# Kernel tuning notes

Measured on AMD Instinct MI355X. Metric: run time of the kernel, lower is better.

Reference implementation:

```python
import jax, jax.numpy as jnp
import numpy as np

N_NODES = 100000
N_EDGES = 3200000


def _gcn_layer(x, W, b, src, dst, n_nodes):
    # GCNConv: x' = D^{-1/2} (A + I) D^{-1/2} X W + b  (self-loops included in src/dst)
    h = x @ W  # [N, F_out]
    ones = jnp.ones(src.shape[0], dtype=x.dtype)
    deg = jax.ops.segment_sum(ones, dst, num_segments=n_nodes)  # in-degree incl. self-loop
    dinv = jnp.where(deg > 0, jax.lax.rsqrt(deg), 0.0)
    norm = dinv[src] * dinv[dst]  # [E+N]
    msg = h[src] * norm[:, None]  # gather + scale
    out = jax.ops.segment_sum(msg, dst, num_segments=n_nodes)  # scatter-add
    return out + b


def setup_inputs() -> dict:
    key = jax.random.key(0)
    k1, k2, k3, k4 = jax.random.split(key, 4)
    x = jax.random.normal(k1, (N_NODES, 64), dtype=jnp.float32)
    edge_index = jax.random.randint(k2, (2, N_EDGES), 0, N_NODES, dtype=jnp.int64)
    W1 = jax.random.normal(k3, (64, 128), dtype=jnp.float32) * (1.0 / np.sqrt(64))
    b1 = jnp.zeros((128,), dtype=jnp.float32)
    W2 = jax.random.normal(k4, (128, 64), dtype=jnp.float32) * (1.0 / np.sqrt(128))
    b2 = jnp.zeros((64,), dtype=jnp.float32)
    return {"x": x, "edge_index": edge_index, "W1": W1, "b1": b1, "W2": W2, "b2": b2}


def reference(x, edge_index, W1, b1, W2, b2):
    n = x.shape[0]
    loop = jnp.arange(n, dtype=edge_index.dtype)
    src = jnp.concatenate([edge_index[0], loop])
    dst = jnp.concatenate([edge_index[1], loop])
    h = _gcn_layer(x, W1, b1, src, dst, n)
    h = jax.nn.relu(h)
    # dropout is identity in eval mode (training=False)
    out = _gcn_layer(h, W2, b2, src, dst, n)
    return out
```

## Files before the change

kernel.cpp:

```cpp
#include <hip/hip_runtime.h>
#include <hip/hip_fp16.h>

#define N_NODES 100000
#define N_EDGES 3200000

#define NBLK_P 320
#define SLICE4 (N_EDGES / 4 / NBLK_P)
#define NBKT 256
#define BSHIFT 9
#define NBKT_USED ((N_NODES + 511) / 512)
#define EL_CAP 24576

struct alignas(8) Half4 { __half2 lo, hi; };


__global__ __launch_bounds__(256) void k_coarse_hist(const int4* __restrict__ dst4,
                                                     int* __restrict__ blockHist) {
    __shared__ int h[NBKT];
    int t = threadIdx.x;
    h[t] = 0;
    __syncthreads();
    int base = blockIdx.x * SLICE4;
    for (int i = t; i < SLICE4; i += 256) {
        int4 d = dst4[base + i];
        atomicAdd(&h[d.x >> BSHIFT], 1);
        atomicAdd(&h[d.y >> BSHIFT], 1);
        atomicAdd(&h[d.z >> BSHIFT], 1);
        atomicAdd(&h[d.w >> BSHIFT], 1);
    }
    __syncthreads();
    blockHist[blockIdx.x * NBKT + t] = h[t];
}

__global__ __launch_bounds__(1024) void k_colscan(int* __restrict__ blockHist,
                                                  int* __restrict__ coarseStart) {
    __shared__ int part[4][NBKT];
    __shared__ int s[NBKT];
    __shared__ int totA[NBKT];
    int tid = threadIdx.x;
    int b = tid & 255, q = tid >> 8;
    const int QR = NBLK_P / 4;
    int sum = 0;
    for (int r = q * QR; r < (q + 1) * QR; ++r) sum += blockHist[r * NBKT + b];
    part[q][b] = sum;
    __syncthreads();
    if (q == 0) {
        int tot = part[0][b] + part[1][b] + part[2][b] + part[3][b];
        s[b] = tot;
        totA[b] = tot;
    }
    __syncthreads();
    for (int off = 1; off < NBKT; off <<= 1) {
        int v = 0;
        if (q == 0 && b >= off) v = s[b - off];
        __syncthreads();
        if (q == 0) s[b] += v;
        __syncthreads();
    }
    int excl = s[b] - totA[b];
    if (q == 0) {
        coarseStart[b] = excl;
        if (b == 0) coarseStart[NBKT] = N_EDGES;
    }
    int run = excl;
    if (q > 0) run += part[0][b];
    if (q > 1) run += part[1][b];
    if (q > 2) run += part[2][b];
    for (int r = q * QR; r < (q + 1) * QR; ++r) {
        int v = blockHist[r * NBKT + b];
        blockHist[r * NBKT + b] = run;
        run += v;
    }
}

__global__ __launch_bounds__(256) void k_partition(const int4* __restrict__ src4,
                                                   const int4* __restrict__ dst4,
                                                   const int* __restrict__ blockHist,
                                                   int* __restrict__ sorted) {
    __shared__ int cur[NBKT];
    int t = threadIdx.x;
    cur[t] = blockHist[blockIdx.x * NBKT + t];
    __syncthreads();
    int base = blockIdx.x * SLICE4;
    for (int i = t; i < SLICE4; i += 256) {
        int4 d = dst4[base + i];
        int4 s = src4[base + i];
        int p;
        p = atomicAdd(&cur[d.x >> BSHIFT], 1); sorted[p] = s.x | ((d.x & 511) << 17);
        p = atomicAdd(&cur[d.y >> BSHIFT], 1); sorted[p] = s.y | ((d.y & 511) << 17);
        p = atomicAdd(&cur[d.z >> BSHIFT], 1); sorted[p] = s.z | ((d.z & 511) << 17);
        p = atomicAdd(&cur[d.w >> BSHIFT], 1); sorted[p] = s.w | ((d.w & 511) << 17);
    }
}

__global__ __launch_bounds__(256) void k_fine(const int* __restrict__ sorted,
                                              const int* __restrict__ coarseStart,
                                              const float4* __restrict__ x4,
                                              int* __restrict__ rowstart,
                                              float* __restrict__ dinvg,
                                              int* __restrict__ csr_src,
                                              Half4* __restrict__ xs) {
    __shared__ int eL[EL_CAP];
    __shared__ int h[512];
    __shared__ int pairsc[256];
    __shared__ int offs[512];
    __shared__ float dloc[512];
    int t = threadIdx.x;
    int bkt = blockIdx.x;
    int beg = coarseStart[bkt], end = coarseStart[bkt + 1];
    int cnt = end - beg;
    bool inLds = (cnt <= EL_CAP);
    h[t] = 0; h[t + 256] = 0;
    __syncthreads();
    if (inLds) {
        for (int i = t; i < cnt; i += 256) eL[i] = sorted[beg + i];
        __syncthreads();
        for (int i = t; i < cnt; i += 256) atomicAdd(&h[eL[i] >> 17], 1);
    } else {
        for (int i = beg + t; i < end; i += 256) atomicAdd(&h[sorted[i] >> 17], 1);
    }
    __syncthreads();
    int pv = h[2 * t] + h[2 * t + 1];
    pairsc[t] = pv;
    __syncthreads();
    for (int off = 1; off < 256; off <<= 1) {
        int v = (t >= off) ? pairsc[t - off] : 0;
        __syncthreads();
        pairsc[t] += v;
        __syncthreads();
    }
    int e0 = pairsc[t] - pv;
    offs[2 * t] = e0;
    offs[2 * t + 1] = e0 + h[2 * t];
    __syncthreads();
    int n0 = bkt << BSHIFT;
    int nvalid = N_NODES - n0;
    if (nvalid > 512) nvalid = 512;
#pragma unroll
    for (int q = 0; q < 2; ++q) {
        int local = t + q * 256;
        if (local < nvalid) {
            rowstart[n0 + local] = beg + offs[local];
            float dv = rsqrtf((float)(h[local] + 1));
            dloc[local] = dv;
            dinvg[n0 + local] = dv;
        }
    }
    if (bkt == 0 && t == 0) rowstart[N_NODES] = N_EDGES;
    __syncthreads();
    if (inLds) {
        for (int i = t; i < cnt; i += 256) {
            int pk = eL[i];
            int p = atomicAdd(&offs[pk >> 17], 1);
            csr_src[beg + p] = pk & 0x1FFFF;
        }
    } else {
        for (int i = beg + t; i < end; i += 256) {
            int pk = sorted[i];
            int p = atomicAdd(&offs[pk >> 17], 1);
            csr_src[beg + p] = pk & 0x1FFFF;
        }
    }
    for (int i = t; i < nvalid * 16; i += 256) {
        int local = i >> 4;
        int qq = i & 15;
        float d = dloc[local];
        float4 v = x4[(long long)(n0 + local) * 16 + qq];
        Half4 hh;
        hh.lo = __float22half2_rn(make_float2(v.x * d, v.y * d));
        hh.hi = __float22half2_rn(make_float2(v.z * d, v.w * d));
        xs[(long long)(n0 + local) * 16 + qq] = hh;
    }
}


__global__ __launch_bounds__(256) void k_gather_h(
    const int* __restrict__ rowstart, const int* __restrict__ csr_src,
    const float* __restrict__ dinv, const int4* __restrict__ xs16,
    const float4* __restrict__ bias4, float4* __restrict__ out4)
{
    int node = blockIdx.x * 4 + (threadIdx.x >> 6);
    if (node >= N_NODES) return;
    int lane = threadIdx.x & 63;
    int qlane = lane & 7;
    int egrp = lane >> 3;
    int beg = rowstart[node];
    int deg = rowstart[node + 1] - beg;
    float acc[8];
#pragma unroll
    for (int k = 0; k < 8; ++k) acc[k] = 0.f;
    if (egrp == 0) {
        int4 v = xs16[((long long)node << 3) + qlane];
        float2 f0 = __half22float2(*(__half2*)&v.x);
        float2 f1 = __half22float2(*(__half2*)&v.y);
        float2 f2 = __half22float2(*(__half2*)&v.z);
        float2 f3 = __half22float2(*(__half2*)&v.w);
        acc[0] = f0.x; acc[1] = f0.y; acc[2] = f1.x; acc[3] = f1.y;
        acc[4] = f2.x; acc[5] = f2.y; acc[6] = f3.x; acc[7] = f3.y;
    }
    for (int base = 0; base < deg; base += 64) {
        int rem = deg - base;
        if (rem > 64) rem = 64;
        int mye = (lane < rem) ? csr_src[beg + base + lane] : 0;
        int nj = (rem + 7) >> 3;
        for (int j = 0; j < nj; ++j) {
            int eidx = (j << 3) + egrp;
            int s = __shfl(mye, eidx);
            if (eidx < rem) {
                int4 v = xs16[((long long)s << 3) + qlane];
                float2 f0 = __half22float2(*(__half2*)&v.x);
                float2 f1 = __half22float2(*(__half2*)&v.y);
                float2 f2 = __half22float2(*(__half2*)&v.z);
                float2 f3 = __half22float2(*(__half2*)&v.w);
                acc[0] += f0.x; acc[1] += f0.y; acc[2] += f1.x; acc[3] += f1.y;
                acc[4] += f2.x; acc[5] += f2.y; acc[6] += f3.x; acc[7] += f3.y;
            }
        }
    }
#pragma unroll
    for (int k = 0; k < 8; ++k) {
        acc[k] += __shfl_xor(acc[k], 8);
        acc[k] += __shfl_xor(acc[k], 16);
        acc[k] += __shfl_xor(acc[k], 32);
    }
    if (egrp == 0) {
        float d = dinv[node];
        float4 b0 = bias4 ? bias4[qlane * 2] : make_float4(0.f, 0.f, 0.f, 0.f);
        float4 b1 = bias4 ? bias4[qlane * 2 + 1] : make_float4(0.f, 0.f, 0.f, 0.f);
        out4[(long long)node * 16 + qlane * 2] =
            make_float4(d * acc[0] + b0.x, d * acc[1] + b0.y, d * acc[2] + b0.z, d * acc[3] + b0.w);
        out4[(long long)node * 16 + qlane * 2 + 1] =
            make_float4(d * acc[4] + b1.x, d * acc[5] + b1.y, d * acc[6] + b1.z, d * acc[7] + b1.w);
    }
}


#define GTILE 128
__global__ __launch_bounds__(256) void k_fused_gemm(
    const float* __restrict__ A, const float* __restrict__ W1,
    const float* __restrict__ b1, const float* __restrict__ W2,
    const float* __restrict__ dinv, Half4* __restrict__ P)
{
    __shared__ float sBuf[128][GTILE];
    int tid = threadIdx.x;
    int R0 = blockIdx.x * GTILE;

    {
        int row = tid >> 1;
        int kb = (tid & 1) * 32;
        int grow = R0 + row;
        if (grow < N_NODES) {
            const float4* src = (const float4*)&A[(long long)grow * 64 + kb];
#pragma unroll
            for (int q = 0; q < 8; ++q) {
                float4 v = src[q];
                int k = kb + q * 4;
                sBuf[k + 0][row] = v.x;
                sBuf[k + 1][row] = v.y;
                sBuf[k + 2][row] = v.z;
                sBuf[k + 3][row] = v.w;
            }
        } else {
#pragma unroll
            for (int q = 0; q < 8; ++q) {
                int k = kb + q * 4;
                sBuf[k + 0][row] = 0.f; sBuf[k + 1][row] = 0.f;
                sBuf[k + 2][row] = 0.f; sBuf[k + 3][row] = 0.f;
            }
        }
    }
    __syncthreads();

    int rg = tid & 15;
    int cg = tid >> 4;
    int r0 = rg * 8;

    float acc[8][8];
#pragma unroll
    for (int i = 0; i < 8; ++i)
#pragma unroll
        for (int j = 0; j < 8; ++j) acc[i][j] = 0.f;
    {
        int c0 = cg * 8;
#pragma unroll 4
        for (int k = 0; k < 64; ++k) {
            float4 a0 = *(const float4*)&sBuf[k][r0];
            float4 a1 = *(const float4*)&sBuf[k][r0 + 4];
            float4 w0 = *(const float4*)&W1[k * 128 + c0];
            float4 w1 = *(const float4*)&W1[k * 128 + c0 + 4];
            float av[8] = {a0.x, a0.y, a0.z, a0.w, a1.x, a1.y, a1.z, a1.w};
            float wv[8] = {w0.x, w0.y, w0.z, w0.w, w1.x, w1.y, w1.z, w1.w};
#pragma unroll
            for (int i = 0; i < 8; ++i)
#pragma unroll
                for (int j = 0; j < 8; ++j) acc[i][j] += av[i] * wv[j];
        }
    }
    __syncthreads();

    {
        int c0 = cg * 8;
#pragma unroll
        for (int j = 0; j < 8; ++j) {
            float bb = b1[c0 + j];
            float4 h0, h1;
            h0.x = fmaxf(acc[0][j] + bb, 0.f);
            h0.y = fmaxf(acc[1][j] + bb, 0.f);
            h0.z = fmaxf(acc[2][j] + bb, 0.f);
            h0.w = fmaxf(acc[3][j] + bb, 0.f);
            h1.x = fmaxf(acc[4][j] + bb, 0.f);
            h1.y = fmaxf(acc[5][j] + bb, 0.f);
            h1.z = fmaxf(acc[6][j] + bb, 0.f);
            h1.w = fmaxf(acc[7][j] + bb, 0.f);
            *(float4*)&sBuf[c0 + j][r0] = h0;
            *(float4*)&sBuf[c0 + j][r0 + 4] = h1;
        }
    }
    __syncthreads();

    {
        int c0 = cg * 4;
        float acc2[8][4];
#pragma unroll
        for (int i = 0; i < 8; ++i)
#pragma unroll
            for (int j = 0; j < 4; ++j) acc2[i][j] = 0.f;
#pragma unroll 4
        for (int k = 0; k < 128; ++k) {
            float4 a0 = *(const float4*)&sBuf[k][r0];
            float4 a1 = *(const float4*)&sBuf[k][r0 + 4];
            float4 w = *(const float4*)&W2[k * 64 + c0];
            float av[8] = {a0.x, a0.y, a0.z, a0.w, a1.x, a1.y, a1.z, a1.w};
            float wv[4] = {w.x, w.y, w.z, w.w};
#pragma unroll
            for (int i = 0; i < 8; ++i)
#pragma unroll
                for (int j = 0; j < 4; ++j) acc2[i][j] += av[i] * wv[j];
        }
#pragma unroll
        for (int i = 0; i < 8; ++i) {
            int row = R0 + r0 + i;
            if (row < N_NODES) {
                float d = dinv[row];
                Half4 h;
                h.lo = __float22half2_rn(make_float2(d * acc2[i][0], d * acc2[i][1]));
                h.hi = __float22half2_rn(make_float2(d * acc2[i][2], d * acc2[i][3]));
                P[(long long)row * 16 + cg] = h;
            }
        }
    }
}


extern "C" void kernel_launch(void* const* d_in, const int* in_sizes, int n_in,
                              void* d_out, int out_size, void* d_ws, size_t ws_size,
                              hipStream_t stream) {
    const float* x  = (const float*)d_in[0];
    const int*   ei = (const int*)d_in[1];
    const float* W1 = (const float*)d_in[2];
    const float* b1 = (const float*)d_in[3];
    const float* W2 = (const float*)d_in[4];
    const float* b2 = (const float*)d_in[5];
    float* out = (float*)d_out;

    const int* srcE = ei;
    const int* dstE = ei + N_EDGES;

    char* w = (char*)d_ws;
    int*   blockHist   = (int*)w;   w += sizeof(int) * NBLK_P * NBKT;
    int*   coarseStart = (int*)w;   w += sizeof(int) * (NBKT + 1);
    int*   rowstart    = (int*)w;   w += sizeof(int) * (N_NODES + 8);
    float* dinv        = (float*)w; w += sizeof(float) * (N_NODES + 8);
    int*   csr_src     = (int*)w;   w += sizeof(int) * N_EDGES;
    Half4* xs          = (Half4*)w; w += sizeof(Half4) * (size_t)N_NODES * 16;
    int*   sorted      = (int*)w;
    float* agg1        = (float*)w; w += sizeof(float) * (size_t)N_NODES * 64;
    Half4* p2 = xs;

    k_coarse_hist<<<NBLK_P, 256, 0, stream>>>((const int4*)dstE, blockHist);
    k_colscan<<<1, 1024, 0, stream>>>(blockHist, coarseStart);
    k_partition<<<NBLK_P, 256, 0, stream>>>((const int4*)srcE, (const int4*)dstE,
                                            blockHist, sorted);
    k_fine<<<NBKT_USED, 256, 0, stream>>>(sorted, coarseStart, (const float4*)x,
                                          rowstart, dinv, csr_src, xs);

    k_gather_h<<<(N_NODES + 3) / 4, 256, 0, stream>>>(rowstart, csr_src, dinv,
                                                      (const int4*)xs, nullptr,
                                                      (float4*)agg1);
    k_fused_gemm<<<(N_NODES + GTILE - 1) / GTILE, 256, 0, stream>>>(agg1, W1, b1, W2, dinv, p2);

    k_gather_h<<<(N_NODES + 3) / 4, 256, 0, stream>>>(rowstart, csr_src, dinv,
                                                      (const int4*)p2, (const float4*)b2,
                                                      (float4*)out);
}
```

Measured before the change: 314.0 us.

## Split gathers into feature halves, store layer-1 aggregate in fp16, use finer buckets

```diff
diff --git a/kernel.cpp b/kernel.cpp
--- a/kernel.cpp
+++ b/kernel.cpp
@@ -6,19 +6,17 @@
 
 #define NBLK_P 320
 #define SLICE4 (N_EDGES / 4 / NBLK_P)
-#define NBKT 256
-#define BSHIFT 9
-#define NBKT_USED ((N_NODES + 511) / 512)
-#define EL_CAP 24576
-
-struct alignas(8) Half4 { __half2 lo, hi; };
+#define NBKT 512
+#define BSHIFT 8
+#define NBKT_USED ((N_NODES + 255) / 256)
+#define EL_CAP 12288
 
 
 __global__ __launch_bounds__(256) void k_coarse_hist(const int4* __restrict__ dst4,
                                                      int* __restrict__ blockHist) {
     __shared__ int h[NBKT];
     int t = threadIdx.x;
-    h[t] = 0;
+    h[t] = 0; h[t + 256] = 0;
     __syncthreads();
     int base = blockIdx.x * SLICE4;
     for (int i = t; i < SLICE4; i += 256) {
@@ -30,22 +28,23 @@
     }
     __syncthreads();
     blockHist[blockIdx.x * NBKT + t] = h[t];
+    blockHist[blockIdx.x * NBKT + t + 256] = h[t + 256];
 }
 
 __global__ __launch_bounds__(1024) void k_colscan(int* __restrict__ blockHist,
                                                   int* __restrict__ coarseStart) {
-    __shared__ int part[4][NBKT];
+    __shared__ int part[2][NBKT];
     __shared__ int s[NBKT];
     __shared__ int totA[NBKT];
     int tid = threadIdx.x;
-    int b = tid & 255, q = tid >> 8;
-    const int QR = NBLK_P / 4;
+    int b = tid & 511, q = tid >> 9;
+    const int QR = NBLK_P / 2;
     int sum = 0;
     for (int r = q * QR; r < (q + 1) * QR; ++r) sum += blockHist[r * NBKT + b];
     part[q][b] = sum;
     __syncthreads();
     if (q == 0) {
-        int tot = part[0][b] + part[1][b] + part[2][b] + part[3][b];
+        int tot = part[0][b] + part[1][b];
         s[b] = tot;
         totA[b] = tot;
     }
@@ -63,9 +62,7 @@
         if (b == 0) coarseStart[NBKT] = N_EDGES;
     }
     int run = excl;
-    if (q > 0) run += part[0][b];
-    if (q > 1) run += part[1][b];
-    if (q > 2) run += part[2][b];
+    if (q == 1) run += part[0][b];
     for (int r = q * QR; r < (q + 1) * QR; ++r) {
         int v = blockHist[r * NBKT + b];
         blockHist[r * NBKT + b] = run;
@@ -80,16 +77,17 @@
     __shared__ int cur[NBKT];
     int t = threadIdx.x;
     cur[t] = blockHist[blockIdx.x * NBKT + t];
+    cur[t + 256] = blockHist[blockIdx.x * NBKT + t + 256];
     __syncthreads();
     int base = blockIdx.x * SLICE4;
     for (int i = t; i < SLICE4; i += 256) {
         int4 d = dst4[base + i];
         int4 s = src4[base + i];
         int p;
-        p = atomicAdd(&cur[d.x >> BSHIFT], 1); sorted[p] = s.x | ((d.x & 511) << 17);
-        p = atomicAdd(&cur[d.y >> BSHIFT], 1); sorted[p] = s.y | ((d.y & 511) << 17);
-        p = atomicAdd(&cur[d.z >> BSHIFT], 1); sorted[p] = s.z | ((d.z & 511) << 17);
-        p = atomicAdd(&cur[d.w >> BSHIFT], 1); sorted[p] = s.w | ((d.w & 511) << 17);
+        p = atomicAdd(&cur[d.x >> BSHIFT], 1); sorted[p] = s.x | ((d.x & 255) << 17);
+        p = atomicAdd(&cur[d.y >> BSHIFT], 1); sorted[p] = s.y | ((d.y & 255) << 17);
+        p = atomicAdd(&cur[d.z >> BSHIFT], 1); sorted[p] = s.z | ((d.z & 255) << 17);
+        p = atomicAdd(&cur[d.w >> BSHIFT], 1); sorted[p] = s.w | ((d.w & 255) << 17);
     }
 }
 
@@ -99,18 +97,18 @@
                                               int* __restrict__ rowstart,
                                               float* __restrict__ dinvg,
                                               int* __restrict__ csr_src,
-                                              Half4* __restrict__ xs) {
+                                              int4* __restrict__ xs) {
     __shared__ int eL[EL_CAP];
-    __shared__ int h[512];
+    __shared__ int h[256];
     __shared__ int pairsc[256];
-    __shared__ int offs[512];
-    __shared__ float dloc[512];
+    __shared__ int offs[256];
+    __shared__ float dloc[256];
     int t = threadIdx.x;
     int bkt = blockIdx.x;
     int beg = coarseStart[bkt], end = coarseStart[bkt + 1];
     int cnt = end - beg;
     bool inLds = (cnt <= EL_CAP);
-    h[t] = 0; h[t + 256] = 0;
+    h[t] = 0;
     __syncthreads();
     if (inLds) {
         for (int i = t; i < cnt; i += 256) eL[i] = sorted[beg + i];
@@ -120,7 +118,7 @@
         for (int i = beg + t; i < end; i += 256) atomicAdd(&h[sorted[i] >> 17], 1);
     }
     __syncthreads();
-    int pv = h[2 * t] + h[2 * t + 1];
+    int pv = h[t];
     pairsc[t] = pv;
     __syncthreads();
     for (int off = 1; off < 256; off <<= 1) {
@@ -130,21 +128,15 @@
         __syncthreads();
     }
     int e0 = pairsc[t] - pv;
-    offs[2 * t] = e0;
-    offs[2 * t + 1] = e0 + h[2 * t];
-    __syncthreads();
+    offs[t] = e0;
     int n0 = bkt << BSHIFT;
     int nvalid = N_NODES - n0;
-    if (nvalid > 512) nvalid = 512;
-#pragma unroll
-    for (int q = 0; q < 2; ++q) {
-        int local = t + q * 256;
-        if (local < nvalid) {
-            rowstart[n0 + local] = beg + offs[local];
-            float dv = rsqrtf((float)(h[local] + 1));
-            dloc[local] = dv;
-            dinvg[n0 + local] = dv;
-        }
+    if (nvalid > 256) nvalid = 256;
+    if (t < nvalid) {
+        rowstart[n0 + t] = beg + e0;
+        float dv = rsqrtf((float)(pv + 1));
+        dloc[t] = dv;
+        dinvg[n0 + t] = dv;
     }
     if (bkt == 0 && t == 0) rowstart[N_NODES] = N_EDGES;
     __syncthreads();
@@ -166,31 +158,28 @@
         int qq = i & 15;
         float d = dloc[local];
         float4 v = x4[(long long)(n0 + local) * 16 + qq];
-        Half4 hh;
-        hh.lo = __float22half2_rn(make_float2(v.x * d, v.y * d));
-        hh.hi = __float22half2_rn(make_float2(v.z * d, v.w * d));
-        xs[(long long)(n0 + local) * 16 + qq] = hh;
-    }
-}
-
-
-__global__ __launch_bounds__(256) void k_gather_h(
+        __half2 lo = __float22half2_rn(make_float2(v.x * d, v.y * d));
+        __half2 hi = __float22half2_rn(make_float2(v.z * d, v.w * d));
+        int4 pk;
+        pk.x = *(int*)&lo;
+        pk.y = *(int*)&hi;
+        ((int2*)xs)[(long long)(n0 + local) * 16 + qq] = make_int2(pk.x, pk.y);
+    }
+}
+
+
+__device__ __forceinline__ void gather_half_core(
     const int* __restrict__ rowstart, const int* __restrict__ csr_src,
-    const float* __restrict__ dinv, const int4* __restrict__ xs16,
-    const float4* __restrict__ bias4, float4* __restrict__ out4)
+    const int4* __restrict__ xs8, int hoff, int node, int lane, float acc[8])
 {
-    int node = blockIdx.x * 4 + (threadIdx.x >> 6);
-    if (node >= N_NODES) return;
-    int lane = threadIdx.x & 63;
-    int qlane = lane & 7;
-    int egrp = lane >> 3;
+    int q = lane & 3;
+    int eg = lane >> 2;
     int beg = rowstart[node];
     int deg = rowstart[node + 1] - beg;
-    float acc[8];
 #pragma unroll
     for (int k = 0; k < 8; ++k) acc[k] = 0.f;
-    if (egrp == 0) {
-        int4 v = xs16[((long long)node << 3) + qlane];
+    if (eg == 0) {
+        int4 v = xs8[((long long)node << 3) + hoff + q];
         float2 f0 = __half22float2(*(__half2*)&v.x);
         float2 f1 = __half22float2(*(__half2*)&v.y);
         float2 f2 = __half22float2(*(__half2*)&v.z);
@@ -202,12 +191,12 @@
         int rem = deg - base;
         if (rem > 64) rem = 64;
         int mye = (lane < rem) ? csr_src[beg + base + lane] : 0;
-        int nj = (rem + 7) >> 3;
+        int nj = (rem + 15) >> 4;
         for (int j = 0; j < nj; ++j) {
-            int eidx = (j << 3) + egrp;
+            int eidx = (j << 4) + eg;
             int s = __shfl(mye, eidx);
             if (eidx < rem) {
-                int4 v = xs16[((long long)s << 3) + qlane];
+                int4 v = xs8[((long long)s << 3) + hoff + q];
                 float2 f0 = __half22float2(*(__half2*)&v.x);
                 float2 f1 = __half22float2(*(__half2*)&v.y);
                 float2 f2 = __half22float2(*(__half2*)&v.z);
@@ -219,17 +208,53 @@
     }
 #pragma unroll
     for (int k = 0; k < 8; ++k) {
+        acc[k] += __shfl_xor(acc[k], 4);
         acc[k] += __shfl_xor(acc[k], 8);
         acc[k] += __shfl_xor(acc[k], 16);
         acc[k] += __shfl_xor(acc[k], 32);
     }
-    if (egrp == 0) {
+}
+
+__global__ __launch_bounds__(256) void k_gather_half_h16(
+    const int* __restrict__ rowstart, const int* __restrict__ csr_src,
+    const float* __restrict__ dinv, const int4* __restrict__ xs8,
+    int hoff, int4* __restrict__ aggh)
+{
+    int node = blockIdx.x * 4 + (threadIdx.x >> 6);
+    if (node >= N_NODES) return;
+    int lane = threadIdx.x & 63;
+    float acc[8];
+    gather_half_core(rowstart, csr_src, xs8, hoff, node, lane, acc);
+    if ((lane >> 2) == 0) {
         float d = dinv[node];
-        float4 b0 = bias4 ? bias4[qlane * 2] : make_float4(0.f, 0.f, 0.f, 0.f);
-        float4 b1 = bias4 ? bias4[qlane * 2 + 1] : make_float4(0.f, 0.f, 0.f, 0.f);
-        out4[(long long)node * 16 + qlane * 2] =
+        __half2 h0 = __float22half2_rn(make_float2(d * acc[0], d * acc[1]));
+        __half2 h1 = __float22half2_rn(make_float2(d * acc[2], d * acc[3]));
+        __half2 h2 = __float22half2_rn(make_float2(d * acc[4], d * acc[5]));
+        __half2 h3 = __float22half2_rn(make_float2(d * acc[6], d * acc[7]));
+        int4 o;
+        o.x = *(int*)&h0; o.y = *(int*)&h1; o.z = *(int*)&h2; o.w = *(int*)&h3;
+        aggh[((long long)node << 3) + hoff + (lane & 3)] = o;
+    }
+}
+
+__global__ __launch_bounds__(256) void k_gather_half_f32(
+    const int* __restrict__ rowstart, const int* __restrict__ csr_src,
+    const float* __restrict__ dinv, const int4* __restrict__ xs8,
+    int hoff, const float4* __restrict__ bias_h, float4* __restrict__ out4)
+{
+    int node = blockIdx.x * 4 + (threadIdx.x >> 6);
+    if (node >= N_NODES) return;
+    int lane = threadIdx.x & 63;
+    float acc[8];
+    gather_half_core(rowstart, csr_src, xs8, hoff, node, lane, acc);
+    int q = lane & 3;
+    if ((lane >> 2) == 0) {
+        float d = dinv[node];
+        float4 b0 = bias_h[q * 2];
+        float4 b1 = bias_h[q * 2 + 1];
+        out4[(long long)node * 16 + hoff * 2 + q * 2] =
             make_float4(d * acc[0] + b0.x, d * acc[1] + b0.y, d * acc[2] + b0.z, d * acc[3] + b0.w);
-        out4[(long long)node * 16 + qlane * 2 + 1] =
+        out4[(long long)node * 16 + hoff * 2 + q * 2 + 1] =
             make_float4(d * acc[4] + b1.x, d * acc[5] + b1.y, d * acc[6] + b1.z, d * acc[7] + b1.w);
     }
 }
@@ -237,9 +262,9 @@
 
 #define GTILE 128
 __global__ __launch_bounds__(256) void k_fused_gemm(
-    const float* __restrict__ A, const float* __restrict__ W1,
+    const int4* __restrict__ Ah, const float* __restrict__ W1,
     const float* __restrict__ b1, const float* __restrict__ W2,
-    const float* __restrict__ dinv, Half4* __restrict__ P)
+    const float* __restrict__ dinv, int2* __restrict__ P)
 {
     __shared__ float sBuf[128][GTILE];
     int tid = threadIdx.x;
@@ -250,23 +275,22 @@
         int kb = (tid & 1) * 32;
         int grow = R0 + row;
         if (grow < N_NODES) {
-            const float4* src = (const float4*)&A[(long long)grow * 64 + kb];
-#pragma unroll
-            for (int q = 0; q < 8; ++q) {
-                float4 v = src[q];
-                int k = kb + q * 4;
-                sBuf[k + 0][row] = v.x;
-                sBuf[k + 1][row] = v.y;
-                sBuf[k + 2][row] = v.z;
-                sBuf[k + 3][row] = v.w;
+#pragma unroll
+            for (int qq = 0; qq < 4; ++qq) {
+                int4 v = Ah[((long long)grow << 3) + (tid & 1) * 4 + qq];
+                float2 f0 = __half22float2(*(__half2*)&v.x);
+                float2 f1 = __half22float2(*(__half2*)&v.y);
+                float2 f2 = __half22float2(*(__half2*)&v.z);
+                float2 f3 = __half22float2(*(__half2*)&v.w);
+                int k = kb + qq * 8;
+                sBuf[k + 0][row] = f0.x; sBuf[k + 1][row] = f0.y;
+                sBuf[k + 2][row] = f1.x; sBuf[k + 3][row] = f1.y;
+                sBuf[k + 4][row] = f2.x; sBuf[k + 5][row] = f2.y;
+                sBuf[k + 6][row] = f3.x; sBuf[k + 7][row] = f3.y;
             }
         } else {
 #pragma unroll
-            for (int q = 0; q < 8; ++q) {
-                int k = kb + q * 4;
-                sBuf[k + 0][row] = 0.f; sBuf[k + 1][row] = 0.f;
-                sBuf[k + 2][row] = 0.f; sBuf[k + 3][row] = 0.f;
-            }
+            for (int qq = 0; qq < 32; ++qq) sBuf[kb + qq][row] = 0.f;
         }
     }
     __syncthreads();
@@ -342,10 +366,9 @@
             int row = R0 + r0 + i;
             if (row < N_NODES) {
                 float d = dinv[row];
-                Half4 h;
-                h.lo = __float22half2_rn(make_float2(d * acc2[i][0], d * acc2[i][1]));
-                h.hi = __float22half2_rn(make_float2(d * acc2[i][2], d * acc2[i][3]));
-                P[(long long)row * 16 + cg] = h;
+                __half2 lo = __float22half2_rn(make_float2(d * acc2[i][0], d * acc2[i][1]));
+                __half2 hi = __float22half2_rn(make_float2(d * acc2[i][2], d * acc2[i][3]));
+                P[(long long)row * 16 + cg] = make_int2(*(int*)&lo, *(int*)&hi);
             }
         }
     }
@@ -372,10 +395,10 @@
     int*   rowstart    = (int*)w;   w += sizeof(int) * (N_NODES + 8);
     float* dinv        = (float*)w; w += sizeof(float) * (N_NODES + 8);
     int*   csr_src     = (int*)w;   w += sizeof(int) * N_EDGES;
-    Half4* xs          = (Half4*)w; w += sizeof(Half4) * (size_t)N_NODES * 16;
+    int4*  xs          = (int4*)w;  w += 16 * (size_t)N_NODES * 8;
     int*   sorted      = (int*)w;
-    float* agg1        = (float*)w; w += sizeof(float) * (size_t)N_NODES * 64;
-    Half4* p2 = xs;
+    int4*  aggh        = (int4*)w;  w += 16 * (size_t)N_NODES * 8;
+    int4*  p2 = xs;
 
     k_coarse_hist<<<NBLK_P, 256, 0, stream>>>((const int4*)dstE, blockHist);
     k_colscan<<<1, 1024, 0, stream>>>(blockHist, coarseStart);
@@ -384,12 +407,17 @@
     k_fine<<<NBKT_USED, 256, 0, stream>>>(sorted, coarseStart, (const float4*)x,
                                           rowstart, dinv, csr_src, xs);
 
-    k_gather_h<<<(N_NODES + 3) / 4, 256, 0, stream>>>(rowstart, csr_src, dinv,
-                                                      (const int4*)xs, nullptr,
-                                                      (float4*)agg1);
-    k_fused_gemm<<<(N_NODES + GTILE - 1) / GTILE, 256, 0, stream>>>(agg1, W1, b1, W2, dinv, p2);
-
-    k_gather_h<<<(N_NODES + 3) / 4, 256, 0, stream>>>(rowstart, csr_src, dinv,
-                                                      (const int4*)p2, (const float4*)b2,
-                                                      (float4*)out);
-}
+    k_gather_half_h16<<<(N_NODES + 3) / 4, 256, 0, stream>>>(rowstart, csr_src, dinv,
+                                                             xs, 0, aggh);
+    k_gather_half_h16<<<(N_NODES + 3) / 4, 256, 0, stream>>>(rowstart, csr_src, dinv,
+                                                             xs, 4, aggh);
+    k_fused_gemm<<<(N_NODES + GTILE - 1) / GTILE, 256, 0, stream>>>(aggh, W1, b1, W2,
+                                                                    dinv, (int2*)p2);
+
+    k_gather_half_f32<<<(N_NODES + 3) / 4, 256, 0, stream>>>(rowstart, csr_src, dinv,
+                                                             p2, 0, (const float4*)b2,
+                                                             (float4*)out);
+    k_gather_half_f32<<<(N_NODES + 3) / 4, 256, 0, stream>>>(rowstart, csr_src, dinv,
+                                                             p2, 4, (const float4*)b2 + 8,
+                                                             (float4*)out);
+}
```

After: 414.8 us. +32.1%, slower.
